# Optimization experiments

Hardware: AMD Instinct MI355X
Metric: run time of the kernel (lower is better)

The kernel has to match this reference:

```python
import jax, jax.numpy as jnp
import numpy as np

DIM = 1024
ATT_DIM = 1024
N_HEADS = 16
HEAD_DIM = ATT_DIM // N_HEADS


def q_rsqrt_np(x):
    # Quake fast inverse sqrt with one Newton iteration, as in the source.
    y = np.asarray([x], dtype=np.float32)
    x2 = y * np.float32(0.5)
    i = y.view(np.int32)
    i = np.right_shift(i, 1)
    i = np.int32(1597463007) - i
    y = i.view(np.float32)
    y = y * (np.float32(1.5) - x2 * y * y)
    # module casts to half: self.scaling = q_rsqrt(head_dim).half()
    return float(np.float16(y[0]))

SCALING = q_rsqrt_np(HEAD_DIM)


def own_softmax(x):
    # max in fp32, exp in fp32, cast exp to fp16, sum in fp16, divide -> fp16
    maxes = jnp.max(x, axis=-1, keepdims=True)
    x_exp = jnp.exp(x - maxes).astype(jnp.float16)
    x_exp_sum = jnp.sum(x_exp, axis=-1, keepdims=True)
    return x_exp / x_exp_sum


def setup_inputs() -> dict:
    key = jax.random.key(0)
    k1, k2, k3 = jax.random.split(key, 3)
    tgt_len = 2048
    x = jax.random.normal(k1, (tgt_len, DIM), dtype=jnp.float32)
    # nn.Linear weights: [out_features, in_features]
    W_in = jax.random.normal(k2, (3 * ATT_DIM, DIM), dtype=jnp.float32) * (1.0 / np.sqrt(DIM))
    W_out = jax.random.normal(k3, (DIM, ATT_DIM), dtype=jnp.float32) * (1.0 / np.sqrt(ATT_DIM))
    return {"x": x, "W_in": W_in, "W_out": W_out, "tgt_len": tgt_len}


def reference(x, W_in, W_out, tgt_len):
    qkv = x @ W_in.T  # [N, 3*att_dim]
    q, k, v = jnp.split(qkv, 3, axis=-1)
    # [N, H, D] -> [H, N, D]
    q = q.reshape(tgt_len, N_HEADS, HEAD_DIM).transpose(1, 0, 2)
    k = k.reshape(tgt_len, N_HEADS, HEAD_DIM).transpose(1, 0, 2)
    v = v.reshape(tgt_len, N_HEADS, HEAD_DIM).transpose(1, 0, 2)
    scores = jnp.einsum('hnd,hmd->hnm', q, k) * SCALING  # [H, N, N] fp32
    probs = own_softmax(scores)  # fp16
    ctx = jnp.einsum('hnm,hmd->hnd', probs.astype(jnp.float32), v)  # [H, N, D]
    ctx = ctx.transpose(1, 0, 2).reshape(tgt_len, ATT_DIM)
    return ctx @ W_out.T
```

## Files before the change

### kernel.cpp

```cpp
#include <hip/hip_runtime.h>
#include <cstring>
#include <cstdint>

#define TGT 2048
#define NH 16
#define HD 64
#define DIM 1024
#define OD3 3072

typedef _Float16 f16x8 __attribute__((ext_vector_type(8)));
typedef _Float16 f16x4 __attribute__((ext_vector_type(4)));
typedef _Float16 f16x2 __attribute__((ext_vector_type(2)));
typedef float f32x4 __attribute__((ext_vector_type(4)));

__device__ __forceinline__ void gload16(const void* g, void* l) {
  __builtin_amdgcn_global_load_lds(
      (const __attribute__((address_space(1))) unsigned int*)g,
      (__attribute__((address_space(3))) unsigned int*)l, 16, 0, 0);
}

__global__ void cast_all(const float* __restrict__ x, const float* __restrict__ win,
                         const float* __restrict__ wout, _Float16* __restrict__ xh,
                         _Float16* __restrict__ winh, _Float16* __restrict__ wouth) {
  const int NX = TGT * DIM / 8, NW = OD3 * DIM / 8, NO = DIM * DIM / 8;
  int i = blockIdx.x * blockDim.x + threadIdx.x;
  const float* src;
  _Float16* dst;
  int off;
  if (i < NX) { src = x; dst = xh; off = i; }
  else if (i < NX + NW) { src = win; dst = winh; off = i - NX; }
  else if (i < NX + NW + NO) { src = wout; dst = wouth; off = i - NX - NW; }
  else return;
  const float4* p = (const float4*)(src + (size_t)off * 8);
  float4 a = p[0], b = p[1];
  f16x8 o;
  o[0] = (_Float16)a.x; o[1] = (_Float16)a.y; o[2] = (_Float16)a.z; o[3] = (_Float16)a.w;
  o[4] = (_Float16)b.x; o[5] = (_Float16)b.y; o[6] = (_Float16)b.z; o[7] = (_Float16)b.w;
  *(f16x8*)(dst + (size_t)off * 8) = o;
}

__global__ __launch_bounds__(256, 3) void gemm_qkv(
    const _Float16* __restrict__ A, const _Float16* __restrict__ B,
    _Float16* __restrict__ qh, _Float16* __restrict__ kg, _Float16* __restrict__ vg) {
  __shared__ __attribute__((aligned(16))) _Float16 As[2][2048];
  __shared__ __attribute__((aligned(16))) _Float16 Bs[2][4096];
  const int tid = threadIdx.x, lane = tid & 63, w = tid >> 6;
  const int g = lane >> 4, c = lane & 15;
  const int wr = w >> 1, wc = w & 1;
  const int id = blockIdx.x;
  const int swz = (id & 7) * 96 + (id >> 3);
  const int bm = (swz / 24) * 64, bn = (swz % 24) * 128;
  f32x4 acc[2][4] = {};

#define QKV_STAGE(buf, k0)                                                              \
  {                                                                                     \
    gload16(A + (size_t)(bm + (tid & 63)) * DIM + (k0) + (tid >> 6) * 8,                \
            &As[buf][tid * 8]);                                                         \
    _Pragma("unroll") for (int t = 0; t < 2; ++t) {                                     \
      int e = t * 256 + tid;                                                            \
      gload16(B + (size_t)(bn + (e & 127)) * DIM + (k0) + (e >> 7) * 8,                 \
              &Bs[buf][e * 8]);                                                         \
    }                                                                                   \
  }

  QKV_STAGE(0, 0);
  __syncthreads();
  for (int kk = 0; kk < 32; ++kk) {
    const int cur = kk & 1;
    if (kk + 1 < 32) QKV_STAGE(cur ^ 1, (kk + 1) * 32);
    f16x8 af[2], bf[4];
#pragma unroll
    for (int m = 0; m < 2; ++m) af[m] = *(const f16x8*)(&As[cur][g * 512 + (wr * 32 + m * 16 + c) * 8]);
#pragma unroll
    for (int n = 0; n < 4; ++n) bf[n] = *(const f16x8*)(&Bs[cur][g * 1024 + (wc * 64 + n * 16 + c) * 8]);
    __builtin_amdgcn_s_setprio(1);
#pragma unroll
    for (int m = 0; m < 2; ++m)
#pragma unroll
      for (int n = 0; n < 4; ++n)
        acc[m][n] = __builtin_amdgcn_mfma_f32_16x16x32_f16(af[m], bf[n], acc[m][n], 0, 0, 0);
    __builtin_amdgcn_s_setprio(0);
    __syncthreads();
  }
#undef QKV_STAGE

  const int which = bn >> 10;
  const int bnn = bn & 1023;
  if (which == 0) {
#pragma unroll
    for (int m = 0; m < 2; ++m)
#pragma unroll
      for (int n = 0; n < 4; ++n)
#pragma unroll
        for (int j = 0; j < 4; ++j) {
          int row = bm + wr * 32 + m * 16 + g * 4 + j;
          int o = bnn + wc * 64 + n * 16 + c;
          qh[((size_t)(o >> 6) * TGT + row) * HD + (o & 63)] = (_Float16)acc[m][n][j];
        }
  } else if (which == 1) {
#pragma unroll
    for (int m = 0; m < 2; ++m)
#pragma unroll
      for (int n = 0; n < 4; ++n)
#pragma unroll
        for (int j = 0; j < 4; ++j) {
          int krow = bm + wr * 32 + m * 16 + g * 4 + j;
          int o = bnn + wc * 64 + n * 16 + c;
          int hh = o >> 6, d = o & 63;
          int kt = krow >> 6, r = krow & 63;
          int blk = (r >> 4) * 2 + (d >> 5);
          int ln = (r & 15) + 16 * ((d >> 3) & 3);
          kg[(size_t)hh * 131072 + kt * 4096 + (blk * 64 + ln) * 8 + (d & 7)] =
              (_Float16)acc[m][n][j];
        }
  } else {
#pragma unroll
    for (int m = 0; m < 2; ++m)
#pragma unroll
      for (int n = 0; n < 4; ++n) {
        int krow0 = bm + wr * 32 + m * 16 + g * 4;
        int o = bnn + wc * 64 + n * 16 + c;
        int hh = o >> 6, d = o & 63;
        int kt = krow0 >> 6, k = krow0 & 63;
        int np = d >> 4, cc = d & 15;
        int ks2 = k >> 5, gg = (k >> 2) & 3, e0 = 4 * ((k >> 4) & 1);
        f16x4 v;
#pragma unroll
        for (int j = 0; j < 4; ++j) v[j] = (_Float16)acc[m][n][j];
        *(f16x4*)(vg + (size_t)hh * 131072 + kt * 4096 +
                  ((np * 2 + ks2) * 64 + cc + 16 * gg) * 8 + e0) = v;
      }
  }
}

__global__ __launch_bounds__(256, 2) void gemm_out(
    const _Float16* __restrict__ A, const _Float16* __restrict__ B, float* __restrict__ out) {
  __shared__ __attribute__((aligned(16))) _Float16 As[2][2048];
  __shared__ __attribute__((aligned(16))) _Float16 Bs[2][2048];
  const int tid = threadIdx.x, lane = tid & 63, w = tid >> 6;
  const int g = lane >> 4, c = lane & 15;
  const int wr = w >> 1, wc = w & 1;
  const int id = blockIdx.x;
  const int swz = (id & 7) * 64 + (id >> 3);
  const int bm = (swz / 16) * 64, bn = (swz % 16) * 64;
  f32x4 acc[2][2] = {};

#define OUT_STAGE(buf, k0)                                                              \
  {                                                                                     \
    gload16(A + (size_t)(bm + (tid & 63)) * DIM + (k0) + (tid >> 6) * 8,                \
            &As[buf][tid * 8]);                                                         \
    gload16(B + (size_t)(bn + (tid & 63)) * DIM + (k0) + (tid >> 6) * 8,                \
            &Bs[buf][tid * 8]);                                                         \
  }

  OUT_STAGE(0, 0);
  __syncthreads();
  for (int kk = 0; kk < 32; ++kk) {
    const int cur = kk & 1;
    if (kk + 1 < 32) OUT_STAGE(cur ^ 1, (kk + 1) * 32);
    f16x8 af[2], bf[2];
#pragma unroll
    for (int m = 0; m < 2; ++m) af[m] = *(const f16x8*)(&As[cur][g * 512 + (wr * 32 + m * 16 + c) * 8]);
#pragma unroll
    for (int n = 0; n < 2; ++n) bf[n] = *(const f16x8*)(&Bs[cur][g * 512 + (wc * 32 + n * 16 + c) * 8]);
    __builtin_amdgcn_s_setprio(1);
#pragma unroll
    for (int m = 0; m < 2; ++m)
#pragma unroll
      for (int n = 0; n < 2; ++n)
        acc[m][n] = __builtin_amdgcn_mfma_f32_16x16x32_f16(af[m], bf[n], acc[m][n], 0, 0, 0);
    __builtin_amdgcn_s_setprio(0);
    __syncthreads();
  }
#undef OUT_STAGE

#pragma unroll
  for (int m = 0; m < 2; ++m)
#pragma unroll
    for (int n = 0; n < 2; ++n)
#pragma unroll
      for (int j = 0; j < 4; ++j) {
        int row = bm + wr * 32 + m * 16 + g * 4 + j;
        int o = bn + wc * 32 + n * 16 + c;
        out[(size_t)row * DIM + o] = acc[m][n][j];
      }
}

__global__ __launch_bounds__(256, 4) void attn(
    const _Float16* __restrict__ qh, const _Float16* __restrict__ kg,
    const _Float16* __restrict__ vg, float* __restrict__ po, float* __restrict__ pml,
    float scal2) {
  __shared__ __attribute__((aligned(16))) _Float16 Ks[2][4096];
  __shared__ __attribute__((aligned(16))) _Float16 Vs[2][4096];
  const int tid = threadIdx.x, lane = tid & 63, w = tid >> 6;
  const int g = lane >> 4, c = lane & 15;
  const int h = blockIdx.y, qblk = blockIdx.x, ks0 = blockIdx.z;
  const int qrow = qblk * 64 + w * 16 + c;
  const _Float16* kb = kg + (size_t)h * 131072 + (size_t)ks0 * 65536;
  const _Float16* vb = vg + (size_t)h * 131072 + (size_t)ks0 * 65536;

  f16x8 qf[2];
#pragma unroll
  for (int ks = 0; ks < 2; ++ks)
    qf[ks] = *(const f16x8*)(qh + ((size_t)h * TGT + qrow) * HD + ks * 32 + g * 8);

  float m2 = -INFINITY, lsum = 0.f;
  f32x4 oacc[4] = {};

#define ATTN_STAGE(buf, kt)                                                    \
  {                                                                            \
    _Pragma("unroll") for (int t = 0; t < 2; ++t) {                            \
      int chunk = t * 256 + tid;                                               \
      gload16(kb + (size_t)(kt) * 4096 + chunk * 8, &Ks[buf][chunk * 8]);      \
      gload16(vb + (size_t)(kt) * 4096 + chunk * 8, &Vs[buf][chunk * 8]);      \
    }                                                                          \
  }

  ATTN_STAGE(0, 0);
  __syncthreads();

  for (int kt = 0; kt < 16; ++kt) {
    const int cur = kt & 1;
    if (kt + 1 < 16) ATTN_STAGE(cur ^ 1, kt + 1);

    f32x4 s[4] = {};
    __builtin_amdgcn_s_setprio(1);
#pragma unroll
    for (int n = 0; n < 4; ++n)
#pragma unroll
      for (int ks = 0; ks < 2; ++ks) {
        f16x8 kf = *(const f16x8*)(&Ks[cur][((n * 2 + ks) * 64 + lane) * 8]);
        s[n] = __builtin_amdgcn_mfma_f32_16x16x32_f16(kf, qf[ks], s[n], 0, 0, 0);
      }
    __builtin_amdgcn_s_setprio(0);

    f32x4 m4;
#pragma unroll
    for (int j = 0; j < 4; ++j) m4[j] = fmaxf(fmaxf(s[0][j], s[1][j]), fmaxf(s[2][j], s[3][j]));
    float mx = fmaxf(fmaxf(m4[0], m4[1]), fmaxf(m4[2], m4[3]));
    mx = fmaxf(mx, __shfl_xor(mx, 16));
    mx = fmaxf(mx, __shfl_xor(mx, 32));
    float pmax = mx * scal2;

    if (!__all(pmax <= m2 + 8.f)) {
      float mnew = fmaxf(m2, pmax);
      float alpha = __builtin_amdgcn_exp2f(m2 - mnew);
      m2 = mnew;
      lsum *= alpha;
#pragma unroll
      for (int np = 0; np < 4; ++np)
#pragma unroll
        for (int j = 0; j < 4; ++j) oacc[np][j] *= alpha;
    }

    float tsum = 0.f;
    uint32_t pk[4][2];
#pragma unroll
    for (int n = 0; n < 4; ++n) {
      float p0 = __builtin_amdgcn_exp2f(__builtin_fmaf(s[n][0], scal2, -m2));
      float p1 = __builtin_amdgcn_exp2f(__builtin_fmaf(s[n][1], scal2, -m2));
      float p2 = __builtin_amdgcn_exp2f(__builtin_fmaf(s[n][2], scal2, -m2));
      float p3 = __builtin_amdgcn_exp2f(__builtin_fmaf(s[n][3], scal2, -m2));
      tsum += (p0 + p1) + (p2 + p3);
      auto a = __builtin_amdgcn_cvt_pkrtz(p0, p1);
      auto b = __builtin_amdgcn_cvt_pkrtz(p2, p3);
      memcpy(&pk[n][0], &a, 4);
      memcpy(&pk[n][1], &b, 4);
    }
    tsum += __shfl_xor(tsum, 16);
    tsum += __shfl_xor(tsum, 32);
    lsum += tsum;

#pragma unroll
    for (int ks = 0; ks < 2; ++ks) {
      f16x8 pa;
      memcpy(&pa, &pk[2 * ks][0], 16);
      __builtin_amdgcn_s_setprio(1);
#pragma unroll
      for (int np = 0; np < 4; ++np) {
        f16x8 vbf = *(const f16x8*)(&Vs[cur][((np * 2 + ks) * 64 + lane) * 8]);
        oacc[np] = __builtin_amdgcn_mfma_f32_16x16x32_f16(vbf, pa, oacc[np], 0, 0, 0);
      }
      __builtin_amdgcn_s_setprio(0);
    }
    __syncthreads();
  }
#undef ATTN_STAGE

  const size_t pbase = ((((size_t)ks0 * 16 + h) * 32 + qblk) * 64 + (w * 16 + c)) * 64;
#pragma unroll
  for (int np = 0; np < 4; ++np)
    *(f32x4*)(po + pbase + np * 16 + g * 4) = oacc[np];
  if (g == 0) {
    const size_t sbase = ((((size_t)ks0 * 16 + h) * 32 + qblk) * 64 + (w * 16 + c)) * 2;
    pml[sbase] = m2;
    pml[sbase + 1] = lsum;
  }
}

__global__ void attn_combine(const float* __restrict__ po, const float* __restrict__ pml,
                             _Float16* __restrict__ ctxh) {
  int i = blockIdx.x * blockDim.x + threadIdx.x;
  int dq = i & 3, hq = i >> 2;
  int h = hq & 15, q = hq >> 4;
  int qblk = q >> 6, qr = q & 63;
  size_t s0 = ((((size_t)0 * 16 + h) * 32 + qblk) * 64 + qr) * 2;
  size_t s1 = ((((size_t)1 * 16 + h) * 32 + qblk) * 64 + qr) * 2;
  float m0 = pml[s0], l0 = pml[s0 + 1];
  float m1 = pml[s1], l1 = pml[s1 + 1];
  float m = fmaxf(m0, m1);
  float e0 = __builtin_amdgcn_exp2f(m0 - m);
  float e1 = __builtin_amdgcn_exp2f(m1 - m);
  float inv = 1.0f / (l0 * e0 + l1 * e1);
  size_t o0b = ((((size_t)0 * 16 + h) * 32 + qblk) * 64 + qr) * 64 + dq * 16;
  size_t o1b = ((((size_t)1 * 16 + h) * 32 + qblk) * 64 + qr) * 64 + dq * 16;
  f16x8 o2[2];
#pragma unroll
  for (int t = 0; t < 2; ++t) {
    f32x4 a0 = *(const f32x4*)(po + o0b + t * 8);
    f32x4 a4 = *(const f32x4*)(po + o0b + t * 8 + 4);
    f32x4 b0 = *(const f32x4*)(po + o1b + t * 8);
    f32x4 b4 = *(const f32x4*)(po + o1b + t * 8 + 4);
#pragma unroll
    for (int j = 0; j < 4; ++j) {
      o2[t][j] = (_Float16)((a0[j] * e0 + b0[j] * e1) * inv);
      o2[t][j + 4] = (_Float16)((a4[j] * e0 + b4[j] * e1) * inv);
    }
  }
  _Float16* dst = ctxh + (size_t)q * DIM + h * HD + dq * 16;
  *(f16x8*)(dst) = o2[0];
  *(f16x8*)(dst + 8) = o2[1];
}

static float fp16_round_host(float x) {
  uint32_t u; memcpy(&u, &x, 4);
  uint32_t sign = u & 0x80000000u;
  uint32_t exp = (u >> 23) & 0xff;
  uint32_t m = u & 0x7fffffu;
  uint32_t low = m & 0x1fffu, hi = m >> 13;
  if (low > 0x1000u || (low == 0x1000u && (hi & 1))) hi++;
  if (hi == 0x400u) { hi = 0; exp++; }
  uint32_t r = sign | (exp << 23) | (hi << 13);
  float f; memcpy(&f, &r, 4); return f;
}

extern "C" void kernel_launch(void* const* d_in, const int* in_sizes, int n_in,
                              void* d_out, int out_size, void* d_ws, size_t ws_size,
                              hipStream_t stream) {
  const float* x = (const float*)d_in[0];
  const float* Win = (const float*)d_in[1];
  const float* Wout = (const float*)d_in[2];
  float* out = (float*)d_out;
  char* ws = (char*)d_ws;
  _Float16* xh    = (_Float16*)(ws);
  _Float16* winh  = (_Float16*)(ws + (4ull << 20));
  _Float16* wouth = (_Float16*)(ws + (10ull << 20));
  _Float16* qh    = (_Float16*)(ws + (12ull << 20));
  _Float16* kg    = (_Float16*)(ws + (16ull << 20));
  _Float16* vg    = (_Float16*)(ws + (20ull << 20));
  _Float16* ctxh  = (_Float16*)(ws + (24ull << 20));
  float*    po    = (float*)(ws + (28ull << 20));
  float*    pml   = (float*)(ws + (46ull << 20));

  float y = 64.0f;
  volatile float x2 = 32.0f;
  int ib; memcpy(&ib, &y, 4);
  ib = 1597463007 - (ib >> 1);
  memcpy(&y, &ib, 4);
  volatile float t1 = x2 * y;
  volatile float t2 = t1 * y;
  volatile float t3 = 1.5f - t2;
  y = y * t3;
  const float scaling = fp16_round_host(y);
  const float scal2 = scaling * 1.4426950408889634f;

  const int ncast = (TGT * DIM + OD3 * DIM + DIM * DIM) / 8;
  cast_all<<<(ncast + 255) / 256, 256, 0, stream>>>(x, Win, Wout, xh, winh, wouth);
  gemm_qkv<<<768, 256, 0, stream>>>(xh, winh, qh, kg, vg);
  attn<<<dim3(32, NH, 2), 256, 0, stream>>>(qh, kg, vg, po, pml, scal2);
  attn_combine<<<512, 256, 0, stream>>>(po, pml, ctxh);
  gemm_out<<<512, 256, 0, stream>>>(ctxh, wouth, out);
}
```

Measured before the change: 106.5 us.

## Use 3-stage LDS pipeline with BK=64 in QKV and output GEMMs

Both projection GEMMs move from a double-buffered BK=32 loop to a triple-buffered BK=64 loop. Prefetch now runs two k-tiles ahead, waits use explicit vmcnt counts, and a single s_barrier per iteration replaces the two __syncthreads. This halves the loop trip count and barrier count and should hide global load latency better. The cost is much larger LDS use (72KB for QKV), which forces gemm_qkv down from 3 to 2 waves-per-SIMD in its launch bounds and so lowers occupancy.

```diff
diff --git a/kernel.cpp b/kernel.cpp
--- a/kernel.cpp
+++ b/kernel.cpp
@@ -39,11 +39,11 @@
   *(f16x8*)(dst + (size_t)off * 8) = o;
 }
 
-__global__ __launch_bounds__(256, 3) void gemm_qkv(
+__global__ __launch_bounds__(256, 2) void gemm_qkv(
     const _Float16* __restrict__ A, const _Float16* __restrict__ B,
     _Float16* __restrict__ qh, _Float16* __restrict__ kg, _Float16* __restrict__ vg) {
-  __shared__ __attribute__((aligned(16))) _Float16 As[2][2048];
-  __shared__ __attribute__((aligned(16))) _Float16 Bs[2][4096];
+  __shared__ __attribute__((aligned(16))) _Float16 As[3][4096];
+  __shared__ __attribute__((aligned(16))) _Float16 Bs[3][8192];
   const int tid = threadIdx.x, lane = tid & 63, w = tid >> 6;
   const int g = lane >> 4, c = lane & 15;
   const int wr = w >> 1, wc = w & 1;
@@ -52,35 +52,46 @@
   const int bm = (swz / 24) * 64, bn = (swz % 24) * 128;
   f32x4 acc[2][4] = {};
 
-#define QKV_STAGE(buf, k0)                                                              \
+#define QKV_STAGE(buf, kt)                                                              \
   {                                                                                     \
-    gload16(A + (size_t)(bm + (tid & 63)) * DIM + (k0) + (tid >> 6) * 8,                \
-            &As[buf][tid * 8]);                                                         \
     _Pragma("unroll") for (int t = 0; t < 2; ++t) {                                     \
       int e = t * 256 + tid;                                                            \
-      gload16(B + (size_t)(bn + (e & 127)) * DIM + (k0) + (e >> 7) * 8,                 \
+      gload16(A + (size_t)(bm + (e & 63)) * DIM + (kt) * 64 + (e >> 6) * 8,             \
+              &As[buf][e * 8]);                                                         \
+    }                                                                                   \
+    _Pragma("unroll") for (int t = 0; t < 4; ++t) {                                     \
+      int e = t * 256 + tid;                                                            \
+      gload16(B + (size_t)(bn + (e & 127)) * DIM + (kt) * 64 + (e >> 7) * 8,            \
               &Bs[buf][e * 8]);                                                         \
     }                                                                                   \
   }
 
   QKV_STAGE(0, 0);
-  __syncthreads();
-  for (int kk = 0; kk < 32; ++kk) {
-    const int cur = kk & 1;
-    if (kk + 1 < 32) QKV_STAGE(cur ^ 1, (kk + 1) * 32);
-    f16x8 af[2], bf[4];
-#pragma unroll
-    for (int m = 0; m < 2; ++m) af[m] = *(const f16x8*)(&As[cur][g * 512 + (wr * 32 + m * 16 + c) * 8]);
-#pragma unroll
-    for (int n = 0; n < 4; ++n) bf[n] = *(const f16x8*)(&Bs[cur][g * 1024 + (wc * 64 + n * 16 + c) * 8]);
-    __builtin_amdgcn_s_setprio(1);
-#pragma unroll
-    for (int m = 0; m < 2; ++m)
+  QKV_STAGE(1, 1);
+  for (int kk = 0; kk < 16; ++kk) {
+    if (kk < 15) asm volatile("s_waitcnt vmcnt(6)" ::: "memory");
+    else         asm volatile("s_waitcnt vmcnt(0)" ::: "memory");
+    __builtin_amdgcn_sched_barrier(0);
+    __builtin_amdgcn_s_barrier();
+    if (kk + 2 < 16) { const int nb = (kk + 2) % 3; QKV_STAGE(nb, kk + 2); }
+    const int cur = kk % 3;
+#pragma unroll
+    for (int ks = 0; ks < 2; ++ks) {
+      f16x8 af[2], bf[4];
+#pragma unroll
+      for (int m = 0; m < 2; ++m)
+        af[m] = *(const f16x8*)(&As[cur][((ks * 4 + g) * 64 + wr * 32 + m * 16 + c) * 8]);
 #pragma unroll
       for (int n = 0; n < 4; ++n)
-        acc[m][n] = __builtin_amdgcn_mfma_f32_16x16x32_f16(af[m], bf[n], acc[m][n], 0, 0, 0);
-    __builtin_amdgcn_s_setprio(0);
-    __syncthreads();
+        bf[n] = *(const f16x8*)(&Bs[cur][((ks * 4 + g) * 128 + wc * 64 + n * 16 + c) * 8]);
+      __builtin_amdgcn_s_setprio(1);
+#pragma unroll
+      for (int m = 0; m < 2; ++m)
+#pragma unroll
+        for (int n = 0; n < 4; ++n)
+          acc[m][n] = __builtin_amdgcn_mfma_f32_16x16x32_f16(af[m], bf[n], acc[m][n], 0, 0, 0);
+      __builtin_amdgcn_s_setprio(0);
+    }
   }
 #undef QKV_STAGE
 
@@ -135,8 +146,8 @@
 
 __global__ __launch_bounds__(256, 2) void gemm_out(
     const _Float16* __restrict__ A, const _Float16* __restrict__ B, float* __restrict__ out) {
-  __shared__ __attribute__((aligned(16))) _Float16 As[2][2048];
-  __shared__ __attribute__((aligned(16))) _Float16 Bs[2][2048];
+  __shared__ __attribute__((aligned(16))) _Float16 As[3][4096];
+  __shared__ __attribute__((aligned(16))) _Float16 Bs[3][4096];
   const int tid = threadIdx.x, lane = tid & 63, w = tid >> 6;
   const int g = lane >> 4, c = lane & 15;
   const int wr = w >> 1, wc = w & 1;
@@ -145,32 +156,43 @@
   const int bm = (swz / 16) * 64, bn = (swz % 16) * 64;
   f32x4 acc[2][2] = {};
 
-#define OUT_STAGE(buf, k0)                                                              \
+#define OUT_STAGE(buf, kt)                                                              \
   {                                                                                     \
-    gload16(A + (size_t)(bm + (tid & 63)) * DIM + (k0) + (tid >> 6) * 8,                \
-            &As[buf][tid * 8]);                                                         \
-    gload16(B + (size_t)(bn + (tid & 63)) * DIM + (k0) + (tid >> 6) * 8,                \
-            &Bs[buf][tid * 8]);                                                         \
+    _Pragma("unroll") for (int t = 0; t < 2; ++t) {                                     \
+      int e = t * 256 + tid;                                                            \
+      gload16(A + (size_t)(bm + (e & 63)) * DIM + (kt) * 64 + (e >> 6) * 8,             \
+              &As[buf][e * 8]);                                                         \
+      gload16(B + (size_t)(bn + (e & 63)) * DIM + (kt) * 64 + (e >> 6) * 8,             \
+              &Bs[buf][e * 8]);                                                         \
+    }                                                                                   \
   }
 
   OUT_STAGE(0, 0);
-  __syncthreads();
-  for (int kk = 0; kk < 32; ++kk) {
-    const int cur = kk & 1;
-    if (kk + 1 < 32) OUT_STAGE(cur ^ 1, (kk + 1) * 32);
-    f16x8 af[2], bf[2];
-#pragma unroll
-    for (int m = 0; m < 2; ++m) af[m] = *(const f16x8*)(&As[cur][g * 512 + (wr * 32 + m * 16 + c) * 8]);
-#pragma unroll
-    for (int n = 0; n < 2; ++n) bf[n] = *(const f16x8*)(&Bs[cur][g * 512 + (wc * 32 + n * 16 + c) * 8]);
-    __builtin_amdgcn_s_setprio(1);
-#pragma unroll
-    for (int m = 0; m < 2; ++m)
+  OUT_STAGE(1, 1);
+  for (int kk = 0; kk < 16; ++kk) {
+    if (kk < 15) asm volatile("s_waitcnt vmcnt(4)" ::: "memory");
+    else         asm volatile("s_waitcnt vmcnt(0)" ::: "memory");
+    __builtin_amdgcn_sched_barrier(0);
+    __builtin_amdgcn_s_barrier();
+    if (kk + 2 < 16) { const int nb = (kk + 2) % 3; OUT_STAGE(nb, kk + 2); }
+    const int cur = kk % 3;
+#pragma unroll
+    for (int ks = 0; ks < 2; ++ks) {
+      f16x8 af[2], bf[2];
+#pragma unroll
+      for (int m = 0; m < 2; ++m)
+        af[m] = *(const f16x8*)(&As[cur][((ks * 4 + g) * 64 + wr * 32 + m * 16 + c) * 8]);
 #pragma unroll
       for (int n = 0; n < 2; ++n)
-        acc[m][n] = __builtin_amdgcn_mfma_f32_16x16x32_f16(af[m], bf[n], acc[m][n], 0, 0, 0);
-    __builtin_amdgcn_s_setprio(0);
-    __syncthreads();
+        bf[n] = *(const f16x8*)(&Bs[cur][((ks * 4 + g) * 64 + wc * 32 + n * 16 + c) * 8]);
+      __builtin_amdgcn_s_setprio(1);
+#pragma unroll
+      for (int m = 0; m < 2; ++m)
+#pragma unroll
+        for (int n = 0; n < 2; ++n)
+          acc[m][n] = __builtin_amdgcn_mfma_f32_16x16x32_f16(af[m], bf[n], acc[m][n], 0, 0, 0);
+      __builtin_amdgcn_s_setprio(0);
+    }
   }
 #undef OUT_STAGE
 
```

After: 107.2 us. Within noise of the previous version (+0.7%).
